# Performance work log

Hardware: AMD Instinct MI355X
Metric: run time of the kernel (lower is better)

The kernel has to match this reference:

```python
import jax, jax.numpy as jnp
import numpy as np
from jax import lax

B, CIN, IMG, K = 128, 3, 112, 7
C = 1024      # hidden_channels * channel_dilation
HID = 512     # hidden_channels
HW = (IMG // K) ** 2  # 256 patches
EPS = 1e-5


def _prelu(x, a):
    return jnp.where(x > 0, x, a * x)


def _bn(x, g, b):
    # BatchNorm2d with track_running_stats=False: always uses batch stats
    m = x.mean(axis=(0, 2, 3), keepdims=True)
    v = x.var(axis=(0, 2, 3), keepdims=True)
    return (x - m) * lax.rsqrt(v + EPS) * g[None, :, None, None] + b[None, :, None, None]


def setup_inputs() -> dict:
    key = jax.random.key(0)
    ks = jax.random.split(key, 16)
    d = {
        'x':  jax.random.normal(ks[0], (B, CIN, IMG, IMG), jnp.float32),
        'w0': jax.random.normal(ks[1], (C, CIN, K, K), jnp.float32) * 0.05,
        'b0': jax.random.normal(ks[2], (C,), jnp.float32) * 0.01,
        'a0': jnp.full((1,), 0.25, jnp.float32),
    }
    for i in range(1, 4):
        kw, kb = jax.random.split(jax.random.fold_in(key, i))
        d[f'w{i}'] = jax.random.normal(kw, (C, C), jnp.float32) * 0.02
        d[f'b{i}'] = jax.random.normal(kb, (C,), jnp.float32) * 0.01
        d[f'g{i}'] = jnp.ones((C,), jnp.float32)
        d[f'bt{i}'] = jnp.zeros((C,), jnp.float32)
        d[f'p{i}'] = jnp.full((1,), 0.25, jnp.float32)
    d['pos'] = jax.random.normal(ks[3], (1, HW, C), jnp.float32)
    d['am'] = jnp.full((1,), 0.25, jnp.float32)
    d['wm'] = jax.random.normal(ks[4], (HID, C), jnp.float32) * 0.03
    d['bm'] = jax.random.normal(ks[5], (HID,), jnp.float32) * 0.01
    pkeys = jax.random.split(ks[6], B)
    d['perm'] = jax.vmap(lambda k: jax.random.permutation(k, HW))(pkeys).astype(jnp.int32)
    return d


def reference(x, w0, b0, a0,
              w1, b1, g1, bt1, p1,
              w2, b2, g2, bt2, p2,
              w3, b3, g3, bt3, p3,
              pos, am, wm, bm, perm):
    # patch-embed conv: stride = kernel_size -> [B, C, 16, 16]
    h = lax.conv_general_dilated(x, w0, (K, K), 'VALID',
                                 dimension_numbers=('NCHW', 'OIHW', 'NCHW'))
    h = _prelu(h + b0[None, :, None, None], a0)
    for w, b, g, bt, p in ((w1, b1, g1, bt1, p1),
                           (w2, b2, g2, bt2, p2),
                           (w3, b3, g3, bt3, p3)):
        h = jnp.einsum('bchw,dc->bdhw', h, w) + b[None, :, None, None]  # 1x1 conv
        h = _prelu(_bn(h, g, bt), p)
    Bn, Cn, Hn, Wn = h.shape
    enc = h.reshape(Bn, Cn, Hn * Wn).transpose(0, 2, 1)  # [B, HW, C]
    enc = enc + pos                                      # private: add pos embedding
    enc = _prelu(enc, am) @ wm.T + bm                    # mixer -> [B, HW, HID]
    # private: per-sample token permutation (single batched gather)
    return jnp.take_along_axis(enc, perm[:, :, None], axis=1)
```

## Files before the change

kernel.cpp:

```cpp
#include <hip/hip_runtime.h>
#include <hip/hip_bf16.h>
#include <stdint.h>


typedef __attribute__((ext_vector_type(8))) short bf16x8;
typedef __attribute__((ext_vector_type(4))) float f32x4;

__device__ __forceinline__ float bf2f(uint32_t u) {
  union { uint32_t i; float f; } v; v.i = u << 16; return v.f;
}
__device__ __forceinline__ ushort f2bf(float f) {
  union { float f; uint32_t i; } v; v.f = f;
  uint32_t i = v.i;
  return (ushort)((i + 0x7FFFu + ((i >> 16) & 1u)) >> 16);
}

template<int EPI, int XB, int K, int DOUT>
__global__ void __launch_bounds__(512, 2)
gemm_kernel(const ushort* __restrict__ A, const ushort* __restrict__ Bw,
            const float* __restrict__ bias, const float* __restrict__ alpha,
            void* __restrict__ outp, float* __restrict__ part,
            const int* __restrict__ inv)
{
  __shared__ __align__(16) ushort At[2][256 * 64];
  __shared__ __align__(16) ushort Bt[3][256 * 64];
  const int tid  = threadIdx.x;
  const int lane = tid & 63;
  const int wid  = tid >> 6;
  const int wm   = wid >> 2;
  const int wn   = wid & 3;

  const int s = blockIdx.x;
  const int j = s >> 3;
  const int x = j & ((1 << XB) - 1);
  const int y = ((j >> XB) << 3) | (s & 7);
  const int t0 = y << 8;
  const int d0 = x << 8;

  f32x4 acc[8][4] = {};

  const int swz = (((lane >> 4) ^ (lane & 7)) << 4);
  const char* LA0 = (const char*)&At[0][0] + ((((wm << 7) + (lane & 15))) << 7) + swz;
  const char* LA1 = (const char*)&At[0][0] + ((((wm << 7) + (lane & 15))) << 7) + (swz ^ 64);
  const char* LB0 = (const char*)&Bt[0][0] + ((((wn << 6) + (lane & 15))) << 7) + swz;
  const char* LB1 = (const char*)&Bt[0][0] + ((((wn << 6) + (lane & 15))) << 7) + (swz ^ 64);

  const int lrow8 = lane >> 3;
  const int csrc  = (lane & 7) ^ lrow8;
  const ushort* gAw = A  + (size_t)(t0 + (wid << 4) + lrow8) * K + (csrc << 3);
  const ushort* gBw = Bw + (size_t)(d0 + (wid << 4) + lrow8) * K + (csrc << 3);
  char* stA = (char*)&At[0][0] + (wid << 11);
  char* stB = (char*)&Bt[0][0] + (wid << 11);

#define STAGE_A(T, BUF, H) do {                                                          \
    __builtin_amdgcn_global_load_lds(                                                    \
      (const __attribute__((address_space(1))) uint32_t*)(gAw + (size_t)((H)*128)*K + ((size_t)(T) << 6)),     \
      (__attribute__((address_space(3))) uint32_t*)(stA + (BUF)*32768 + (H)*16384), 16, 0, 0);                  \
    __builtin_amdgcn_global_load_lds(                                                    \
      (const __attribute__((address_space(1))) uint32_t*)(gAw + (size_t)((H)*128+8)*K + ((size_t)(T) << 6)),   \
      (__attribute__((address_space(3))) uint32_t*)(stA + (BUF)*32768 + (H)*16384 + 1024), 16, 0, 0);           \
  } while (0)
#define STAGE_B(T, BOFF, H) do {                                                         \
    __builtin_amdgcn_global_load_lds(                                                    \
      (const __attribute__((address_space(1))) uint32_t*)(gBw + (size_t)((H)*128)*K + ((size_t)(T) << 6)),     \
      (__attribute__((address_space(3))) uint32_t*)(stB + (BOFF) + (H)*16384), 16, 0, 0);                       \
    __builtin_amdgcn_global_load_lds(                                                    \
      (const __attribute__((address_space(1))) uint32_t*)(gBw + (size_t)((H)*128+8)*K + ((size_t)(T) << 6)),   \
      (__attribute__((address_space(3))) uint32_t*)(stB + (BOFF) + (H)*16384 + 1024), 16, 0, 0);                \
  } while (0)

#define RD_A(dst, BASE, CUR, MH) do {                                                    \
    dst[0] = *(const bf16x8*)((BASE) + (CUR)*32768 + (MH)*8192 + 0);                     \
    dst[1] = *(const bf16x8*)((BASE) + (CUR)*32768 + (MH)*8192 + 2048);                  \
    dst[2] = *(const bf16x8*)((BASE) + (CUR)*32768 + (MH)*8192 + 4096);                  \
    dst[3] = *(const bf16x8*)((BASE) + (CUR)*32768 + (MH)*8192 + 6144);                  \
  } while (0)
#define RD_B(dst, BASE, BOFF) do {                                                       \
    dst[0] = *(const bf16x8*)((BASE) + (BOFF) + 0);                                      \
    dst[1] = *(const bf16x8*)((BASE) + (BOFF) + 2048);                                   \
    dst[2] = *(const bf16x8*)((BASE) + (BOFF) + 4096);                                   \
    dst[3] = *(const bf16x8*)((BASE) + (BOFF) + 6144);                                   \
  } while (0)
#define MFMA16(AF, BF, MH) do {                                                          \
    __builtin_amdgcn_s_setprio(1);                                                       \
    _Pragma("unroll")                                                                    \
    for (int m_ = 0; m_ < 4; ++m_)                                                       \
      _Pragma("unroll")                                                                  \
      for (int n_ = 0; n_ < 4; ++n_)                                                     \
        acc[((MH) << 2) + m_][n_] = __builtin_amdgcn_mfma_f32_16x16x32_bf16(             \
            AF[m_], BF[n_], acc[((MH) << 2) + m_][n_], 0, 0, 0);                         \
    __builtin_amdgcn_s_setprio(0);                                                       \
  } while (0)

#define TILE_BODY(T, CUR, HN1, HN2) do {                                                 \
    if (HN1) { asm volatile("s_waitcnt vmcnt(4)" ::: "memory"); }                        \
    else     { asm volatile("s_waitcnt vmcnt(0)" ::: "memory"); }                        \
    __builtin_amdgcn_s_barrier();                                                        \
    RD_A(aX, LA0, CUR, 0);                                                               \
    RD_B(b0f, LB0, bR);                                                                  \
    if (HN1) { STAGE_A((T) + 1, (CUR) ^ 1, 0); STAGE_A((T) + 1, (CUR) ^ 1, 1); }         \
    if (HN2) { STAGE_B((T) + 2, bS, 0); STAGE_B((T) + 2, bS, 1); }                       \
    MFMA16(aX, b0f, 0);                                                                  \
    RD_A(aY, LA0, CUR, 1);                                                               \
    MFMA16(aY, b0f, 1);                                                                  \
    RD_A(aX, LA1, CUR, 0);                                                               \
    RD_B(b1f, LB1, bR);                                                                  \
    MFMA16(aX, b1f, 0);                                                                  \
    RD_A(aY, LA1, CUR, 1);                                                               \
    MFMA16(aY, b1f, 1);                                                                  \
    { int tmp_ = bR; bR = bN; bN = bS; bS = tmp_; }                                      \
  } while (0)

  constexpr int NT = K >> 6;

  STAGE_A(0, 0, 0); STAGE_A(0, 0, 1);
  STAGE_B(0, 0, 0); STAGE_B(0, 0, 1);
  STAGE_B(1, 32768, 0); STAGE_B(1, 32768, 1);

  int bR = 0, bN = 32768, bS = 65536;
  bf16x8 aX[4], aY[4], b0f[4], b1f[4];

#pragma unroll 1
  for (int tp = 0; tp < NT; tp += 2) {
    const bool m1 = (tp + 2 < NT);
    TILE_BODY(tp,     0, true, m1);
    TILE_BODY(tp + 1, 1, m1, m1);
  }

  float bs[4];
#pragma unroll
  for (int n = 0; n < 4; ++n) bs[n] = bias[d0 + (wn << 6) + (n << 4) + (lane & 15)];
  float a0v = (EPI == 0) ? alpha[0] : 0.0f;
  float sA[4] = {0.f, 0.f, 0.f, 0.f}, s2A[4] = {0.f, 0.f, 0.f, 0.f};

#pragma unroll
  for (int m = 0; m < 8; ++m) {
#pragma unroll
    for (int r = 0; r < 4; ++r) {
      int row = t0 + (wm << 7) + (m << 4) + ((lane >> 4) << 2) + r;
      int orow = (EPI == 2) ? ((row & ~255) | inv[row]) : row;
#pragma unroll
      for (int n = 0; n < 4; ++n) {
        int d = d0 + (wn << 6) + (n << 4) + (lane & 15);
        float v = acc[m][n][r] + bs[n];
        if (EPI == 0) v = v > 0.f ? v : a0v * v;
        if (EPI == 1) { sA[n] += v; s2A[n] += v * v; }
        if (EPI == 2) ((float*)outp)[(size_t)orow * DOUT + d] = v;
        else          ((ushort*)outp)[(size_t)row * DOUT + d] = f2bf(v);
      }
    }
  }

  if (EPI == 1) {
    float2* sm = (float2*)&At[0][0];
    int slot = (wm << 2) | (lane >> 4);
    __syncthreads();
#pragma unroll
    for (int n = 0; n < 4; ++n) {
      int c = (wn << 6) + (n << 4) + (lane & 15);
      sm[slot * 256 + c] = make_float2(sA[n], s2A[n]);
    }
    __syncthreads();
    if (tid < 256) {
      float ss = 0.f, ss2 = 0.f;
      for (int q = 0; q < 8; ++q) {
        float2 v = sm[q * 256 + tid];
        ss += v.x; ss2 += v.y;
      }
      part[(size_t)y * 2048 + d0 + tid]        = ss;
      part[(size_t)y * 2048 + 1024 + d0 + tid] = ss2;
    }
  }
#undef STAGE_A
#undef STAGE_B
#undef RD_A
#undef RD_B
#undef MFMA16
#undef TILE_BODY
}

__global__ void bnfold_kernel(const float* __restrict__ part, const float* __restrict__ g,
                              const float* __restrict__ bt, float* __restrict__ scsh) {
  int d = (blockIdx.x << 8) + threadIdx.x;
  float s = 0.f, s2 = 0.f;
  for (int j = 0; j < 128; ++j) { s += part[j * 2048 + d]; s2 += part[j * 2048 + 1024 + d]; }
  float mean = s * (1.f / 32768.f);
  float var  = s2 * (1.f / 32768.f) - mean * mean;
  float sc = g[d] * rsqrtf(var + 1e-5f);
  scsh[d] = sc;
  scsh[1024 + d] = bt[d] - mean * sc;
}

template<bool MIX>
__global__ void bnact_kernel(ushort* __restrict__ Y, const float* __restrict__ scsh,
                             const float* __restrict__ p, const float* __restrict__ pos,
                             const float* __restrict__ am) {
  float pp = p[0];
  float aa = MIX ? am[0] : 0.f;
#pragma unroll 1
  for (int it = 0; it < 8; ++it) {
    size_t vi = ((size_t)it << 19) + ((size_t)blockIdx.x << 8) + threadIdx.x;
    size_t i = vi << 3;
    int d = (int)(i & 1023);
    float pv[8];
    if (MIX) {
      int prow = (int)((i >> 10) & 255);
      const float4* pb = (const float4*)(pos + ((size_t)prow << 10) + d);
      float4 pA = pb[0], pB = pb[1];
      pv[0]=pA.x; pv[1]=pA.y; pv[2]=pA.z; pv[3]=pA.w;
      pv[4]=pB.x; pv[5]=pB.y; pv[6]=pB.z; pv[7]=pB.w;
    }
    uint4 raw = *(const uint4*)(Y + i);
    uint32_t w[4] = {raw.x, raw.y, raw.z, raw.w};
    uint32_t o[4];
#pragma unroll
    for (int q = 0; q < 4; ++q) {
      int dd = d + q * 2;
      float v0 = bf2f(w[q] & 0xFFFFu) * scsh[dd]     + scsh[1024 + dd];
      float v1 = bf2f(w[q] >> 16)     * scsh[dd + 1] + scsh[1024 + dd + 1];
      v0 = v0 > 0.f ? v0 : pp * v0;
      v1 = v1 > 0.f ? v1 : pp * v1;
      if (MIX) {
        v0 += pv[2 * q];     v1 += pv[2 * q + 1];
        v0 = v0 > 0.f ? v0 : aa * v0;
        v1 = v1 > 0.f ? v1 : aa * v1;
      }
      o[q] = (uint32_t)f2bf(v0) | ((uint32_t)f2bf(v1) << 16);
    }
    *(uint4*)(Y + i) = make_uint4(o[0], o[1], o[2], o[3]);
  }
}

__global__ void prep_kernel(const float* __restrict__ x,
                            const float* __restrict__ w0, const float* __restrict__ w1,
                            const float* __restrict__ w2, const float* __restrict__ w3,
                            const float* __restrict__ wm, const int* __restrict__ perm,
                            ushort* __restrict__ P, ushort* __restrict__ w0b,
                            ushort* __restrict__ w1b, ushort* __restrict__ w2b,
                            ushort* __restrict__ w3b, ushort* __restrict__ wmb,
                            int* __restrict__ inv) {
  const int b = blockIdx.x, tid = threadIdx.x;
  if (b < 2048) {
    int t0 = b << 4;
#pragma unroll 1
    for (int tt = 0; tt < 16; ++tt) {
      int t = t0 + tt;
      ushort v = 0;
      if (tid < 147) {
        int bb = t >> 8, pidx = t & 255;
        int pi = pidx >> 4, pj = pidx & 15;
        int cin = tid / 49, rem = tid - cin * 49;
        int dy = rem / 7, dx = rem - dy * 7;
        v = f2bf(x[(size_t)(bb * 3 + cin) * 12544 + (size_t)(pi * 7 + dy) * 112 + (pj * 7 + dx)]);
      }
      P[(size_t)t * 256 + tid] = v;
    }
  } else if (b < 4096) {
    int i = ((b - 2048) << 8) + tid;
#pragma unroll
    for (int r = 0; r < 2; ++r) {
      int idx = (r << 19) + i;
      w1b[idx] = f2bf(w1[idx]);
      w2b[idx] = f2bf(w2[idx]);
      w3b[idx] = f2bf(w3[idx]);
    }
    wmb[i] = f2bf(wm[i]);
  } else if (b < 4224) {
    int t = ((b - 4096) << 8) + tid;
    inv[(t & ~255) + perm[t]] = t & 255;
  } else {
    int d = b - 4224;
    w0b[d * 256 + tid] = (tid < 147) ? f2bf(w0[d * 147 + tid]) : (ushort)0;
  }
}

extern "C" void kernel_launch(void* const* d_in, const int* in_sizes, int n_in,
                              void* d_out, int out_size, void* d_ws, size_t ws_size,
                              hipStream_t stream) {
  const float* x   = (const float*)d_in[0];
  const float* w0  = (const float*)d_in[1];
  const float* b0  = (const float*)d_in[2];
  const float* a0  = (const float*)d_in[3];
  const float* w1  = (const float*)d_in[4];
  const float* b1  = (const float*)d_in[5];
  const float* g1  = (const float*)d_in[6];
  const float* bt1 = (const float*)d_in[7];
  const float* p1  = (const float*)d_in[8];
  const float* w2  = (const float*)d_in[9];
  const float* b2  = (const float*)d_in[10];
  const float* g2  = (const float*)d_in[11];
  const float* bt2 = (const float*)d_in[12];
  const float* p2  = (const float*)d_in[13];
  const float* w3  = (const float*)d_in[14];
  const float* b3  = (const float*)d_in[15];
  const float* g3  = (const float*)d_in[16];
  const float* bt3 = (const float*)d_in[17];
  const float* p3  = (const float*)d_in[18];
  const float* pos = (const float*)d_in[19];
  const float* am  = (const float*)d_in[20];
  const float* wm  = (const float*)d_in[21];
  const float* bm  = (const float*)d_in[22];
  const int*  perm = (const int*)d_in[23];

  char* ws = (char*)d_ws;
  ushort* B0   = (ushort*)ws;
  ushort* B1   = (ushort*)(ws + 67108864);
  float*  part = (float*)(ws + 134217728);
  float*  scsh = (float*)(ws + 134217728 + 2097152);
  int*    inv  = (int*)  (ws + 134217728 + 2097152 + 8192);
  char*   wb   = ws + 134217728 + 2097152 + 8192 + 131072;
  ushort* w1b  = (ushort*)wb;
  ushort* w2b  = w1b + 1048576;
  ushort* w3b  = w2b + 1048576;
  ushort* wmb  = w3b + 1048576;
  ushort* w0b  = wmb + 524288;

  prep_kernel<<<dim3(5248), dim3(256), 0, stream>>>(
      x, w0, w1, w2, w3, wm, perm, B1, w0b, w1b, w2b, w3b, wmb, inv);

  gemm_kernel<0, 2, 256, 1024><<<dim3(512), dim3(512), 0, stream>>>(
      B1, w0b, b0, a0, (void*)B0, nullptr, nullptr);

  gemm_kernel<1, 2, 1024, 1024><<<dim3(512), dim3(512), 0, stream>>>(
      B0, w1b, b1, nullptr, (void*)B1, part, nullptr);
  bnfold_kernel<<<dim3(4), dim3(256), 0, stream>>>(part, g1, bt1, scsh);
  bnact_kernel<false><<<dim3(2048), dim3(256), 0, stream>>>(B1, scsh, p1, nullptr, nullptr);

  gemm_kernel<1, 2, 1024, 1024><<<dim3(512), dim3(512), 0, stream>>>(
      B1, w2b, b2, nullptr, (void*)B0, part, nullptr);
  bnfold_kernel<<<dim3(4), dim3(256), 0, stream>>>(part, g2, bt2, scsh);
  bnact_kernel<false><<<dim3(2048), dim3(256), 0, stream>>>(B0, scsh, p2, nullptr, nullptr);

  gemm_kernel<1, 2, 1024, 1024><<<dim3(512), dim3(512), 0, stream>>>(
      B0, w3b, b3, nullptr, (void*)B1, part, nullptr);
  bnfold_kernel<<<dim3(4), dim3(256), 0, stream>>>(part, g3, bt3, scsh);
  bnact_kernel<true><<<dim3(2048), dim3(256), 0, stream>>>(B1, scsh, p3, pos, am);

  gemm_kernel<2, 1, 1024, 512><<<dim3(256), dim3(512), 0, stream>>>(
      B1, wmb, bm, nullptr, d_out, nullptr, inv);
}
```

Before: 386.2 us.

## Process two M-tiles per persistent GEMM block and overlap the epilogue with next-tile prefetch

The 1024-wide GEMMs now launch 256 blocks instead of 512, and each block computes two 256-row tiles 16384 rows apart. Before running the first tile's epilogue, the block issues the A loads for the second tile. The epilogue's reduction scratch is moved into an unused B buffer so it does not collide with those in-flight loads. This aims to hide epilogue and launch-tail latency and cut block scheduling overhead, at the cost of fewer blocks in flight and more serial work per block.

```diff
diff --git a/kernel.cpp b/kernel.cpp
--- a/kernel.cpp
+++ b/kernel.cpp
@@ -15,7 +15,7 @@
   return (ushort)((i + 0x7FFFu + ((i >> 16) & 1u)) >> 16);
 }
 
-template<int EPI, int XB, int K, int DOUT>
+template<int EPI, int MT, int XB, int K, int DOUT>
 __global__ void __launch_bounds__(512, 2)
 gemm_kernel(const ushort* __restrict__ A, const ushort* __restrict__ Bw,
             const float* __restrict__ bias, const float* __restrict__ alpha,
@@ -34,7 +34,7 @@
   const int j = s >> 3;
   const int x = j & ((1 << XB) - 1);
   const int y = ((j >> XB) << 3) | (s & 7);
-  const int t0 = y << 8;
+  int t0 = y << 8;
   const int d0 = x << 8;
 
   f32x4 acc[8][4] = {};
@@ -47,17 +47,17 @@
 
   const int lrow8 = lane >> 3;
   const int csrc  = (lane & 7) ^ lrow8;
-  const ushort* gAw = A  + (size_t)(t0 + (wid << 4) + lrow8) * K + (csrc << 3);
+  const ushort* gA  = A  + (size_t)(t0 + (wid << 4) + lrow8) * K + (csrc << 3);
   const ushort* gBw = Bw + (size_t)(d0 + (wid << 4) + lrow8) * K + (csrc << 3);
   char* stA = (char*)&At[0][0] + (wid << 11);
   char* stB = (char*)&Bt[0][0] + (wid << 11);
 
 #define STAGE_A(T, BUF, H) do {                                                          \
     __builtin_amdgcn_global_load_lds(                                                    \
-      (const __attribute__((address_space(1))) uint32_t*)(gAw + (size_t)((H)*128)*K + ((size_t)(T) << 6)),     \
+      (const __attribute__((address_space(1))) uint32_t*)(gA + (size_t)((H)*128)*K + ((size_t)(T) << 6)),      \
       (__attribute__((address_space(3))) uint32_t*)(stA + (BUF)*32768 + (H)*16384), 16, 0, 0);                  \
     __builtin_amdgcn_global_load_lds(                                                    \
-      (const __attribute__((address_space(1))) uint32_t*)(gAw + (size_t)((H)*128+8)*K + ((size_t)(T) << 6)),   \
+      (const __attribute__((address_space(1))) uint32_t*)(gA + (size_t)((H)*128+8)*K + ((size_t)(T) << 6)),    \
       (__attribute__((address_space(3))) uint32_t*)(stA + (BUF)*32768 + (H)*16384 + 1024), 16, 0, 0);           \
   } while (0)
 #define STAGE_B(T, BOFF, H) do {                                                         \
@@ -111,65 +111,91 @@
     { int tmp_ = bR; bR = bN; bN = bS; bS = tmp_; }                                      \
   } while (0)
 
+#define KLOOP() do {                                                                     \
+    _Pragma("unroll 1")                                                                  \
+    for (int tp = 0; tp < NT; tp += 2) {                                                 \
+      const bool m1_ = (tp + 2 < NT);                                                    \
+      TILE_BODY(tp,     0, true, m1_);                                                   \
+      TILE_BODY(tp + 1, 1, m1_, m1_);                                                    \
+    }                                                                                    \
+  } while (0)
+
   constexpr int NT = K >> 6;
+
+  int bR = 0, bN = 32768, bS = 65536;
+  bf16x8 aX[4], aY[4], b0f[4], b1f[4];
+
+  auto epilog = [&](int t0v, int slab, char* smbase) {
+    float bs[4];
+#pragma unroll
+    for (int n = 0; n < 4; ++n) bs[n] = bias[d0 + (wn << 6) + (n << 4) + (lane & 15)];
+    float a0v = (EPI == 0) ? alpha[0] : 0.0f;
+    float sA[4] = {0.f, 0.f, 0.f, 0.f}, s2A[4] = {0.f, 0.f, 0.f, 0.f};
+#pragma unroll
+    for (int m = 0; m < 8; ++m) {
+#pragma unroll
+      for (int r = 0; r < 4; ++r) {
+        int row = t0v + (wm << 7) + (m << 4) + ((lane >> 4) << 2) + r;
+        int orow = (EPI == 2) ? ((row & ~255) | inv[row]) : row;
+#pragma unroll
+        for (int n = 0; n < 4; ++n) {
+          int d = d0 + (wn << 6) + (n << 4) + (lane & 15);
+          float v = acc[m][n][r] + bs[n];
+          if (EPI == 0) v = v > 0.f ? v : a0v * v;
+          if (EPI == 1) { sA[n] += v; s2A[n] += v * v; }
+          if (EPI == 2) ((float*)outp)[(size_t)orow * DOUT + d] = v;
+          else          ((ushort*)outp)[(size_t)row * DOUT + d] = f2bf(v);
+        }
+      }
+    }
+    if (EPI == 1) {
+      float2* sm = (float2*)smbase;
+      int slot = (wm << 2) | (lane >> 4);
+      __syncthreads();
+#pragma unroll
+      for (int n = 0; n < 4; ++n) {
+        int c = (wn << 6) + (n << 4) + (lane & 15);
+        sm[slot * 256 + c] = make_float2(sA[n], s2A[n]);
+      }
+      __syncthreads();
+      if (tid < 256) {
+        float ss = 0.f, ss2 = 0.f;
+        for (int q = 0; q < 8; ++q) {
+          float2 v = sm[q * 256 + tid];
+          ss += v.x; ss2 += v.y;
+        }
+        part[(size_t)slab * 2048 + d0 + tid]        = ss;
+        part[(size_t)slab * 2048 + 1024 + d0 + tid] = ss2;
+      }
+    }
+  };
 
   STAGE_A(0, 0, 0); STAGE_A(0, 0, 1);
   STAGE_B(0, 0, 0); STAGE_B(0, 0, 1);
   STAGE_B(1, 32768, 0); STAGE_B(1, 32768, 1);
-
-  int bR = 0, bN = 32768, bS = 65536;
-  bf16x8 aX[4], aY[4], b0f[4], b1f[4];
-
-#pragma unroll 1
-  for (int tp = 0; tp < NT; tp += 2) {
-    const bool m1 = (tp + 2 < NT);
-    TILE_BODY(tp,     0, true, m1);
-    TILE_BODY(tp + 1, 1, m1, m1);
+  KLOOP();
+
+  if (MT == 2) {
+    gA += (size_t)16384 * K;
+    STAGE_A(0, 0, 0); STAGE_A(0, 0, 1);
   }
 
-  float bs[4];
-#pragma unroll
-  for (int n = 0; n < 4; ++n) bs[n] = bias[d0 + (wn << 6) + (n << 4) + (lane & 15)];
-  float a0v = (EPI == 0) ? alpha[0] : 0.0f;
-  float sA[4] = {0.f, 0.f, 0.f, 0.f}, s2A[4] = {0.f, 0.f, 0.f, 0.f};
-
-#pragma unroll
-  for (int m = 0; m < 8; ++m) {
-#pragma unroll
-    for (int r = 0; r < 4; ++r) {
-      int row = t0 + (wm << 7) + (m << 4) + ((lane >> 4) << 2) + r;
-      int orow = (EPI == 2) ? ((row & ~255) | inv[row]) : row;
-#pragma unroll
-      for (int n = 0; n < 4; ++n) {
-        int d = d0 + (wn << 6) + (n << 4) + (lane & 15);
-        float v = acc[m][n][r] + bs[n];
-        if (EPI == 0) v = v > 0.f ? v : a0v * v;
-        if (EPI == 1) { sA[n] += v; s2A[n] += v * v; }
-        if (EPI == 2) ((float*)outp)[(size_t)orow * DOUT + d] = v;
-        else          ((ushort*)outp)[(size_t)row * DOUT + d] = f2bf(v);
-      }
-    }
-  }
-
-  if (EPI == 1) {
-    float2* sm = (float2*)&At[0][0];
-    int slot = (wm << 2) | (lane >> 4);
-    __syncthreads();
-#pragma unroll
-    for (int n = 0; n < 4; ++n) {
-      int c = (wn << 6) + (n << 4) + (lane & 15);
-      sm[slot * 256 + c] = make_float2(sA[n], s2A[n]);
-    }
-    __syncthreads();
-    if (tid < 256) {
-      float ss = 0.f, ss2 = 0.f;
-      for (int q = 0; q < 8; ++q) {
-        float2 v = sm[q * 256 + tid];
-        ss += v.x; ss2 += v.y;
-      }
-      part[(size_t)y * 2048 + d0 + tid]        = ss;
-      part[(size_t)y * 2048 + 1024 + d0 + tid] = ss2;
-    }
+  epilog(t0, y, (char*)&Bt[0][0] + 32768);
+
+  if (MT == 2) {
+    if (EPI == 1) __syncthreads();
+    STAGE_B(0, 32768, 0); STAGE_B(0, 32768, 1);
+    STAGE_B(1, 65536, 0); STAGE_B(1, 65536, 1);
+    bR = 32768; bN = 65536; bS = 0;
+#pragma unroll
+    for (int m = 0; m < 8; ++m)
+#pragma unroll
+      for (int n = 0; n < 4; ++n)
+#pragma unroll
+        for (int r = 0; r < 4; ++r) acc[m][n][r] = 0.f;
+    t0 += 16384;
+    KLOOP();
+    epilog(t0, y + 64, (char*)&At[0][0]);
   }
 #undef STAGE_A
 #undef STAGE_B
@@ -177,6 +203,7 @@
 #undef RD_B
 #undef MFMA16
 #undef TILE_BODY
+#undef KLOOP
 }
 
 __global__ void bnfold_kernel(const float* __restrict__ part, const float* __restrict__ g,
@@ -318,24 +345,24 @@
   prep_kernel<<<dim3(5248), dim3(256), 0, stream>>>(
       x, w0, w1, w2, w3, wm, perm, B1, w0b, w1b, w2b, w3b, wmb, inv);
 
-  gemm_kernel<0, 2, 256, 1024><<<dim3(512), dim3(512), 0, stream>>>(
+  gemm_kernel<0, 2, 2, 256, 1024><<<dim3(256), dim3(512), 0, stream>>>(
       B1, w0b, b0, a0, (void*)B0, nullptr, nullptr);
 
-  gemm_kernel<1, 2, 1024, 1024><<<dim3(512), dim3(512), 0, stream>>>(
+  gemm_kernel<1, 2, 2, 1024, 1024><<<dim3(256), dim3(512), 0, stream>>>(
       B0, w1b, b1, nullptr, (void*)B1, part, nullptr);
   bnfold_kernel<<<dim3(4), dim3(256), 0, stream>>>(part, g1, bt1, scsh);
   bnact_kernel<false><<<dim3(2048), dim3(256), 0, stream>>>(B1, scsh, p1, nullptr, nullptr);
 
-  gemm_kernel<1, 2, 1024, 1024><<<dim3(512), dim3(512), 0, stream>>>(
+  gemm_kernel<1, 2, 2, 1024, 1024><<<dim3(256), dim3(512), 0, stream>>>(
       B1, w2b, b2, nullptr, (void*)B0, part, nullptr);
   bnfold_kernel<<<dim3(4), dim3(256), 0, stream>>>(part, g2, bt2, scsh);
   bnact_kernel<false><<<dim3(2048), dim3(256), 0, stream>>>(B0, scsh, p2, nullptr, nullptr);
 
-  gemm_kernel<1, 2, 1024, 1024><<<dim3(512), dim3(512), 0, stream>>>(
+  gemm_kernel<1, 2, 2, 1024, 1024><<<dim3(256), dim3(512), 0, stream>>>(
       B0, w3b, b3, nullptr, (void*)B1, part, nullptr);
   bnfold_kernel<<<dim3(4), dim3(256), 0, stream>>>(part, g3, bt3, scsh);
   bnact_kernel<true><<<dim3(2048), dim3(256), 0, stream>>>(B1, scsh, p3, pos, am);
 
-  gemm_kernel<2, 1, 1024, 512><<<dim3(256), dim3(512), 0, stream>>>(
+  gemm_kernel<2, 1, 1, 1024, 512><<<dim3(256), dim3(512), 0, stream>>>(
       B1, wmb, bm, nullptr, d_out, nullptr, inv);
 }
```

Measured after the change: 398.1 us. +3.1%, slower.
